# Kernel tuning notes

Hardware: AMD Instinct MI355X
Metric: run time of the kernel (lower is better)

## Reference

```python
import jax, jax.numpy as jnp
import numpy as np
from jax import lax

H = W = 128
V = 16   # object_types
A = 8    # action_types
P = 64   # num_programs
C = 3    # input_channels
MAX_TIMEOUT = 50
DIRS = jnp.array([(1,0),(0,1),(-1,0),(0,-1),(1,1),(-1,1),(1,-1),(-1,-1)], dtype=jnp.int32)


def setup_inputs() -> dict:
    key = jax.random.key(0)
    ks = jax.random.split(key, 9)
    return {
        "obs": jax.random.normal(ks[0], (C, H, W), jnp.float32),
        "conv_w": jax.random.normal(ks[1], (V, C, 3, 3), jnp.float32) * 0.1,
        "conv_b": jax.random.normal(ks[2], (V,), jnp.float32) * 0.1,
        "w_obj": jax.random.normal(ks[3], (P, V), jnp.float32),
        "w_pos": jax.random.normal(ks[4], (P, V), jnp.float32),
        "w_neg": jax.random.normal(ks[5], (P, V), jnp.float32),
        "w_act": jax.random.normal(ks[6], (P, A), jnp.float32),
        "w_dir": jax.random.normal(ks[7], (P, 8), jnp.float32),
        "w_not": jax.random.normal(ks[8], (P, 2), jnp.float32),
    }


def reference(obs, conv_w, conv_b, w_obj, w_pos, w_neg, w_act, w_dir, w_not):
    # --- EntityExtractor: conv -> argmax over channels -> [H,W] object-id grid ---
    x = lax.conv_general_dilated(obs[None], conv_w, (1, 1), 'SAME',
                                 dimension_numbers=('NCHW', 'OIHW', 'NCHW'))
    grid = jnp.argmax(x[0] + conv_b[:, None, None], axis=0).astype(jnp.int32)  # [H,W]

    # first (row-major) occurrence of each object value, per at_cell_with_value/argwhere
    flat = grid.reshape(-1)                                   # [H*W]
    masks = flat[None, :] == jnp.arange(V, dtype=jnp.int32)[:, None]  # [V, H*W]
    exists = masks.any(axis=1)                                # [V]
    first = jnp.argmax(masks, axis=1).astype(jnp.int32)       # [V]
    fr, fc = first // W, first % W

    HW = H * W
    skey = jax.random.key(42)
    k1, k2, k3, k4, k5, k6 = jax.random.split(skey, 6)
    # one categorical sample per (cell, program) call, per-program logits
    def samp(k, logits):
        return jax.random.categorical(k, logits[None], shape=(HW, P)).reshape(-1)  # [N]
    s_obj = samp(k1, w_obj)
    s_pos = samp(k2, w_pos)
    s_neg = samp(k3, w_neg)
    s_act = samp(k4, w_act)
    s_dir = samp(k5, w_dir)
    s_not = samp(k6, w_not)

    r0 = fr[s_obj]                     # [N] start cell = first cell holding s_obj
    c0 = fc[s_obj]
    ex = exists[s_obj]                 # cell is None if object absent
    dr = DIRS[s_dir, 0]
    dc = DIRS[s_dir, 1]

    t = jnp.arange(1, MAX_TIMEOUT + 1, dtype=jnp.int32)       # [T]
    rs = r0[:, None] + t[None, :] * dr[:, None]               # [N,T]
    cs = c0[:, None] + t[None, :] * dc[:, None]
    inb = (rs >= 0) & (cs >= 0) & (rs < H) & (cs < W)
    vals = grid[jnp.clip(rs, 0, H - 1), jnp.clip(cs, 0, W - 1)]
    hit_pos = inb & (vals == s_pos[:, None])                  # true_condition
    stop = hit_pos | (inb & (vals == s_neg[:, None])) | ~inb  # any terminating event
    has = stop.any(axis=1)
    ft = jnp.argmax(stop, axis=1)                             # first event index
    cond = ex & has & jnp.take_along_axis(hit_pos, ft[:, None], axis=1)[:, 0]
    cond = cond ^ (s_not == 1)                                # is_not flip

    counts = jax.ops.segment_sum(cond.astype(jnp.float32), s_act, num_segments=A)
    return jax.nn.softmax(counts)
```

## Files before the change

### kernel.cpp

```cpp
#include <hip/hip_runtime.h>
#include <stdint.h>
#include <math.h>

#define Hh 128
#define Ww 128
#define Vn 16
#define An 8
#define Pn 64
#define Cn 3
#define HWc (Hh*Ww)
#define MAXT 50
#define NB 16

__constant__ int c_DR[8] = {1, 0, -1, 0, 1, -1, 1, -1};
__constant__ int c_DC[8] = {0, 1, 0, -1, 1, 1, -1, -1};

__device__ __forceinline__ void softmaxS(const float* __restrict__ w,
                                         float* __restrict__ o, int n, int os) {
  float m = -INFINITY;
  for (int i = 0; i < n; ++i) m = fmaxf(m, w[i]);
  float s = 0.f;
  for (int i = 0; i < n; ++i) { float e = expf(w[i] - m); o[i * os] = e; s += e; }
  float inv = 1.f / s;
  for (int i = 0; i < n; ++i) o[i * os] *= inv;
}

__global__ __launch_bounds__(1024) void k_prep(const float* __restrict__ obs,
                                               const float* __restrict__ cw,
                                               const float* __restrict__ cb,
                                               uint8_t* __restrict__ grid8,
                                               int* __restrict__ bf) {
  __shared__ float sw[Vn * Cn * 9];
  __shared__ float sb[Vn];
  __shared__ int lf[Vn];
  int t = threadIdx.x;
  for (int i = t; i < Vn * Cn * 9; i += 1024) sw[i] = cw[i];
  if (t < Vn) { sb[t] = cb[t]; lf[t] = 0; }
  __syncthreads();

  int cell = blockIdx.x * 1024 + t;
  int r = cell >> 7, c = cell & 127;
  float o[27];
#pragma unroll
  for (int ch = 0; ch < Cn; ++ch)
#pragma unroll
    for (int ky = 0; ky < 3; ++ky)
#pragma unroll
      for (int kx = 0; kx < 3; ++kx) {
        int rr = r + ky - 1, cc = c + kx - 1;
        o[ch * 9 + ky * 3 + kx] =
            ((unsigned)rr < (unsigned)Hh && (unsigned)cc < (unsigned)Ww)
                ? obs[(ch * Hh + rr) * Ww + cc] : 0.f;
      }
  float best = -INFINITY; int bi = 0;
#pragma unroll
  for (int v = 0; v < Vn; ++v) {
    float acc = sb[v];
#pragma unroll
    for (int i = 0; i < 27; ++i) acc += o[i] * sw[v * 27 + i];
    if (acc > best) { best = acc; bi = v; }
  }
  grid8[cell] = (uint8_t)bi;
  atomicMax(&lf[bi], HWc - cell);
  __syncthreads();
  if (t < Vn) bf[blockIdx.x * Vn + t] = lf[t];
}

__global__ __launch_bounds__(1024) void k_mid(const uint8_t* __restrict__ grid8g,
                                              const int* __restrict__ bf,
                                              const float* __restrict__ w_obj,
                                              const float* __restrict__ w_pos,
                                              const float* __restrict__ w_neg,
                                              const float* __restrict__ w_dir,
                                              float* __restrict__ qPart) {
  __shared__ uint8_t g8[HWc];
  __shared__ float2 sPPN[16 * 64];
  __shared__ float PObjT[16 * 64];
  __shared__ float PDirT[8 * 64];
  __shared__ uint32_t Ftab32[8 * 4];
  __shared__ uint32_t idxLo[8], idxHi[8], finM[8];
  __shared__ float qod[8 * 64];
  __shared__ int sEx[Vn], sFr[Vn], sFc[Vn];

  int t = threadIdx.x;
  int blk = blockIdx.x;
  int wave = t >> 6, lane = t & 63;

  ((uint4*)g8)[t] = ((const uint4*)grid8g)[t];
  if (t < Vn) {
    int m = 0;
#pragma unroll
    for (int b = 0; b < NB; ++b) m = max(m, bf[b * Vn + t]);
    int ex = (m >= 1);
    sEx[t] = ex;
    int cell = ex ? (HWc - m) : 0;
    sFr[t] = cell >> 7;
    sFc[t] = cell & 127;
  }
  {
    int p = lane;
    if      (wave == 0) softmaxS(w_obj + p * 16, &PObjT[p], 16, 64);
    else if (wave == 1) softmaxS(w_pos + p * 16, &((float*)sPPN)[p * 2],     16, 128);
    else if (wave == 2) softmaxS(w_neg + p * 16, &((float*)sPPN)[p * 2 + 1], 16, 128);
    else if (wave == 3) softmaxS(w_dir + p * 8,  &PDirT[p], 8, 64);
  }
  __syncthreads();

  if (wave < 8) {
    int so = blk, sd = wave;
    int step = lane + 1;
    int val = 255;
    if (step <= MAXT && sEx[so]) {
      int r = sFr[so] + step * c_DR[sd];
      int c = sFc[so] + step * c_DC[sd];
      if ((unsigned)r < (unsigned)Hh && (unsigned)c < (unsigned)Ww)
        val = g8[(r << 7) + c];
    }
    uint8_t* Fb = (uint8_t*)Ftab32;
#pragma unroll
    for (int v = 0; v < Vn; ++v) {
      unsigned long long m = __ballot(val == v);
      if (lane == v) Fb[wave * 16 + v] = m ? (uint8_t)__builtin_ctzll(m) : (uint8_t)64;
    }
  }
  __syncthreads();

  if (t < 8) {
    int F[16];
#pragma unroll
    for (int k = 0; k < 4; ++k) {
      uint32_t w = Ftab32[t * 4 + k];
#pragma unroll
      for (int b = 0; b < 4; ++b) F[k * 4 + b] = (w >> (8 * b)) & 0xFF;
    }
    uint32_t lo = 0, hi = 0, fm = 0;
#pragma unroll
    for (int v = 0; v < 16; ++v) {
      int rk = 0;
#pragma unroll
      for (int n = 0; n < 16; ++n)
        if (n != v) rk += (F[n] > F[v]) || (F[n] == F[v] && n < v);
      if (rk < 8) lo |= (uint32_t)v << (4 * rk);
      else        hi |= (uint32_t)v << (4 * (rk - 8));
      fm |= (F[v] < 64 ? 1u : 0u) << rk;
    }
    idxLo[t] = lo; idxHi[t] = hi; finM[t] = fm;
  }
  __syncthreads();

  if (wave < 8) {
    uint32_t lo = idxLo[wave], hi = idxHi[wave], fm = finM[wave];
    float acc = 0.f, inner = 0.f;
#pragma unroll
    for (int r = 0; r < 16; ++r) {
      uint32_t i = ((r < 8) ? (lo >> (4 * r)) : (hi >> (4 * (r - 8)))) & 15u;
      float2 pn = sPPN[i * 64 + lane];
      acc += pn.y;
      inner = fmaf(((fm >> r) & 1u) ? pn.x : 0.f, acc, inner);
    }
    qod[wave * 64 + lane] = PObjT[blk * 64 + lane] * PDirT[wave * 64 + lane] * inner;
  }
  __syncthreads();
  if (t < 64) {
    float s = 0.f;
#pragma unroll
    for (int w = 0; w < 8; ++w) s += qod[w * 64 + t];
    qPart[blk * 64 + t] = s;
  }
}

__global__ __launch_bounds__(64) void k_last(const float* __restrict__ qPart,
                                             const float* __restrict__ w_act,
                                             const float* __restrict__ w_not,
                                             float* __restrict__ out) {
  __shared__ float sAct[64 * 8];
  __shared__ float sNot[64 * 2];
  __shared__ float sCnt[An];
  int t = threadIdx.x;
  if (t < An) sCnt[t] = 0.f;
  softmaxS(w_act + t * 8, &sAct[t * 8], 8, 1);
  softmaxS(w_not + t * 2, &sNot[t * 2], 2, 1);
  __syncthreads();

  float q = 0.f;
#pragma unroll
  for (int b = 0; b < NB; ++b) q += qPart[b * 64 + t];
  float r = q * sNot[t * 2] + (1.f - q) * sNot[t * 2 + 1];
  float scale = 16384.f * r;
#pragma unroll
  for (int a = 0; a < 8; ++a)
    atomicAdd(&sCnt[a], scale * sAct[t * 8 + a]);
  __syncthreads();

  if (t < An) {
    float m = -INFINITY;
    float c[An];
#pragma unroll
    for (int i = 0; i < An; ++i) { c[i] = sCnt[i]; m = fmaxf(m, c[i]); }
    float s = 0.f;
#pragma unroll
    for (int i = 0; i < An; ++i) s += expf(c[i] - m);
    out[t] = expf(c[t] - m) / s;
  }
}

extern "C" void kernel_launch(void* const* d_in, const int* in_sizes, int n_in,
                              void* d_out, int out_size, void* d_ws, size_t ws_size,
                              hipStream_t stream) {
  const float* obs    = (const float*)d_in[0];
  const float* conv_w = (const float*)d_in[1];
  const float* conv_b = (const float*)d_in[2];
  const float* w_obj  = (const float*)d_in[3];
  const float* w_pos  = (const float*)d_in[4];
  const float* w_neg  = (const float*)d_in[5];
  const float* w_act  = (const float*)d_in[6];
  const float* w_dir  = (const float*)d_in[7];
  const float* w_not  = (const float*)d_in[8];
  float* out = (float*)d_out;

  uint8_t* ws = (uint8_t*)d_ws;
  int*     bf    = (int*)(ws + 0);
  uint8_t* grid8 = ws + 1024;
  float*   qPart = (float*)(ws + 1024 + 16384);

  k_prep<<<dim3(NB), dim3(1024), 0, stream>>>(obs, conv_w, conv_b, grid8, bf);
  k_mid<<<dim3(NB), dim3(1024), 0, stream>>>(grid8, bf, w_obj, w_pos, w_neg,
                                             w_dir, qPart);
  k_last<<<dim3(1), dim3(64), 0, stream>>>(qPart, w_act, w_not, out);
}
```

Baseline: 100.1 us.

## Fuse final reduction into middle kernel via last-block atomic counter; widen prep grid

Removes the third kernel launch by having the last finishing block of the middle kernel, detected with a global atomic counter, perform the cross-block sum, the action/not softmax weighting, and the final softmax using wave shuffles. The prep kernel now runs 64 blocks of 256 threads instead of 16 of 1024, which spreads the convolution across more CUs. The per-block first-occurrence maxima are reduced with shared atomics. This saves a launch and its dependency gap, at the cost of threadfence and atomic synchronisation and a counter that must be reset on every call.

```diff
diff --git a/kernel.cpp b/kernel.cpp
--- a/kernel.cpp
+++ b/kernel.cpp
@@ -11,6 +11,7 @@
 #define HWc (Hh*Ww)
 #define MAXT 50
 #define NB 16
+#define PB 64
 
 __constant__ int c_DR[8] = {1, 0, -1, 0, 1, -1, 1, -1};
 __constant__ int c_DC[8] = {0, 1, 0, -1, 1, 1, -1, -1};
@@ -25,20 +26,22 @@
   for (int i = 0; i < n; ++i) o[i * os] *= inv;
 }
 
-__global__ __launch_bounds__(1024) void k_prep(const float* __restrict__ obs,
-                                               const float* __restrict__ cw,
-                                               const float* __restrict__ cb,
-                                               uint8_t* __restrict__ grid8,
-                                               int* __restrict__ bf) {
+__global__ __launch_bounds__(256) void k_prep(const float* __restrict__ obs,
+                                              const float* __restrict__ cw,
+                                              const float* __restrict__ cb,
+                                              uint8_t* __restrict__ grid8,
+                                              int* __restrict__ bf,
+                                              uint32_t* __restrict__ done) {
   __shared__ float sw[Vn * Cn * 9];
   __shared__ float sb[Vn];
   __shared__ int lf[Vn];
   int t = threadIdx.x;
-  for (int i = t; i < Vn * Cn * 9; i += 1024) sw[i] = cw[i];
+  for (int i = t; i < Vn * Cn * 9; i += 256) sw[i] = cw[i];
   if (t < Vn) { sb[t] = cb[t]; lf[t] = 0; }
-  __syncthreads();
-
-  int cell = blockIdx.x * 1024 + t;
+  if (blockIdx.x == 0 && t == 0) *done = 0u;
+  __syncthreads();
+
+  int cell = blockIdx.x * 256 + t;
   int r = cell >> 7, c = cell & 127;
   float o[27];
 #pragma unroll
@@ -66,43 +69,53 @@
   if (t < Vn) bf[blockIdx.x * Vn + t] = lf[t];
 }
 
-__global__ __launch_bounds__(1024) void k_mid(const uint8_t* __restrict__ grid8g,
-                                              const int* __restrict__ bf,
-                                              const float* __restrict__ w_obj,
-                                              const float* __restrict__ w_pos,
-                                              const float* __restrict__ w_neg,
-                                              const float* __restrict__ w_dir,
-                                              float* __restrict__ qPart) {
+__global__ __launch_bounds__(1024) void k_tail(const uint8_t* __restrict__ grid8g,
+                                               const int* __restrict__ bf,
+                                               const float* __restrict__ w_obj,
+                                               const float* __restrict__ w_pos,
+                                               const float* __restrict__ w_neg,
+                                               const float* __restrict__ w_dir,
+                                               const float* __restrict__ w_act,
+                                               const float* __restrict__ w_not,
+                                               float* __restrict__ qPart,
+                                               uint32_t* __restrict__ done,
+                                               float* __restrict__ out) {
   __shared__ uint8_t g8[HWc];
   __shared__ float2 sPPN[16 * 64];
   __shared__ float PObjT[16 * 64];
   __shared__ float PDirT[8 * 64];
+  __shared__ float sAct[64 * 8];
+  __shared__ float sNot[64 * 2];
   __shared__ uint32_t Ftab32[8 * 4];
   __shared__ uint32_t idxLo[8], idxHi[8], finM[8];
   __shared__ float qod[8 * 64];
-  __shared__ int sEx[Vn], sFr[Vn], sFc[Vn];
+  __shared__ int lf16[Vn], sEx[Vn], sFr[Vn], sFc[Vn];
 
   int t = threadIdx.x;
   int blk = blockIdx.x;
   int wave = t >> 6, lane = t & 63;
 
   ((uint4*)g8)[t] = ((const uint4*)grid8g)[t];
-  if (t < Vn) {
-    int m = 0;
-#pragma unroll
-    for (int b = 0; b < NB; ++b) m = max(m, bf[b * Vn + t]);
-    int ex = (m >= 1);
-    sEx[t] = ex;
-    int cell = ex ? (HWc - m) : 0;
-    sFr[t] = cell >> 7;
-    sFc[t] = cell & 127;
-  }
+  if (t < Vn) lf16[t] = 0;
+  __syncthreads();
+  atomicMax(&lf16[t & 15], bf[t]);
   {
     int p = lane;
     if      (wave == 0) softmaxS(w_obj + p * 16, &PObjT[p], 16, 64);
     else if (wave == 1) softmaxS(w_pos + p * 16, &((float*)sPPN)[p * 2],     16, 128);
     else if (wave == 2) softmaxS(w_neg + p * 16, &((float*)sPPN)[p * 2 + 1], 16, 128);
     else if (wave == 3) softmaxS(w_dir + p * 8,  &PDirT[p], 8, 64);
+    else if (wave == 4) softmaxS(w_act + p * 8,  &sAct[p * 8], 8, 1);
+    else if (wave == 5) softmaxS(w_not + p * 2,  &sNot[p * 2], 2, 1);
+  }
+  __syncthreads();
+  if (t < Vn) {
+    int m = lf16[t];
+    int ex = (m >= 1);
+    sEx[t] = ex;
+    int cell = ex ? (HWc - m) : 0;
+    sFr[t] = cell >> 7;
+    sFc[t] = cell & 127;
   }
   __syncthreads();
 
@@ -161,46 +174,43 @@
     qod[wave * 64 + lane] = PObjT[blk * 64 + lane] * PDirT[wave * 64 + lane] * inner;
   }
   __syncthreads();
-  if (t < 64) {
+
+  if (wave == 0) {
     float s = 0.f;
 #pragma unroll
-    for (int w = 0; w < 8; ++w) s += qod[w * 64 + t];
-    qPart[blk * 64 + t] = s;
-  }
-}
-
-__global__ __launch_bounds__(64) void k_last(const float* __restrict__ qPart,
-                                             const float* __restrict__ w_act,
-                                             const float* __restrict__ w_not,
-                                             float* __restrict__ out) {
-  __shared__ float sAct[64 * 8];
-  __shared__ float sNot[64 * 2];
-  __shared__ float sCnt[An];
-  int t = threadIdx.x;
-  if (t < An) sCnt[t] = 0.f;
-  softmaxS(w_act + t * 8, &sAct[t * 8], 8, 1);
-  softmaxS(w_not + t * 2, &sNot[t * 2], 2, 1);
-  __syncthreads();
-
-  float q = 0.f;
-#pragma unroll
-  for (int b = 0; b < NB; ++b) q += qPart[b * 64 + t];
-  float r = q * sNot[t * 2] + (1.f - q) * sNot[t * 2 + 1];
-  float scale = 16384.f * r;
-#pragma unroll
-  for (int a = 0; a < 8; ++a)
-    atomicAdd(&sCnt[a], scale * sAct[t * 8 + a]);
-  __syncthreads();
-
-  if (t < An) {
-    float m = -INFINITY;
-    float c[An];
-#pragma unroll
-    for (int i = 0; i < An; ++i) { c[i] = sCnt[i]; m = fmaxf(m, c[i]); }
-    float s = 0.f;
-#pragma unroll
-    for (int i = 0; i < An; ++i) s += expf(c[i] - m);
-    out[t] = expf(c[t] - m) / s;
+    for (int w = 0; w < 8; ++w) s += qod[w * 64 + lane];
+    qPart[blk * 64 + lane] = s;
+
+    __threadfence();
+    uint32_t old = 0;
+    if (lane == 0) old = atomicAdd(done, 1u);
+    old = __shfl(old, 0, 64);
+    if (old == (uint32_t)(NB - 1)) {
+      __threadfence();
+      float q = 0.f;
+#pragma unroll
+      for (int b = 0; b < NB; ++b)
+        q += __hip_atomic_load(&qPart[b * 64 + lane],
+                               __ATOMIC_RELAXED, __HIP_MEMORY_SCOPE_AGENT);
+      float r = q * sNot[lane * 2] + (1.f - q) * sNot[lane * 2 + 1];
+      float scale = 16384.f * r;
+      float c[An];
+#pragma unroll
+      for (int a = 0; a < An; ++a) {
+        float va = scale * sAct[lane * 8 + a];
+#pragma unroll
+        for (int off = 32; off >= 1; off >>= 1)
+          va += __shfl_down(va, off, 64);
+        c[a] = __shfl(va, 0, 64);
+      }
+      float m = -INFINITY;
+#pragma unroll
+      for (int a = 0; a < An; ++a) m = fmaxf(m, c[a]);
+      float s2 = 0.f;
+#pragma unroll
+      for (int a = 0; a < An; ++a) s2 += expf(c[a] - m);
+      if (lane < An) out[lane] = expf(c[lane] - m) / s2;
+    }
   }
 }
 
@@ -219,12 +229,12 @@
   float* out = (float*)d_out;
 
   uint8_t* ws = (uint8_t*)d_ws;
-  int*     bf    = (int*)(ws + 0);
-  uint8_t* grid8 = ws + 1024;
-  float*   qPart = (float*)(ws + 1024 + 16384);
-
-  k_prep<<<dim3(NB), dim3(1024), 0, stream>>>(obs, conv_w, conv_b, grid8, bf);
-  k_mid<<<dim3(NB), dim3(1024), 0, stream>>>(grid8, bf, w_obj, w_pos, w_neg,
-                                             w_dir, qPart);
-  k_last<<<dim3(1), dim3(64), 0, stream>>>(qPart, w_act, w_not, out);
-}
+  int*      bf    = (int*)(ws + 0);
+  uint8_t*  grid8 = ws + 4096;
+  float*    qPart = (float*)(ws + 4096 + 16384);
+  uint32_t* done  = (uint32_t*)(ws + 4096 + 16384 + 4096);
+
+  k_prep<<<dim3(PB), dim3(256), 0, stream>>>(obs, conv_w, conv_b, grid8, bf, done);
+  k_tail<<<dim3(NB), dim3(1024), 0, stream>>>(grid8, bf, w_obj, w_pos, w_neg,
+                                              w_dir, w_act, w_not, qPart, done, out);
+}
```

Result: faster. 81.98 us, median of 2 (-18.1%).
